# Kernel tuning notes

Hardware: AMD Instinct MI355X
Metric: run time of the kernel (lower is better)

Reference implementation:

```python
import jax, jax.numpy as jnp
import numpy as np

IMG_H, IMG_W = 512.0, 512.0
PRE_NMS = 2000   # training-mode pre_nms_top_n
POST_NMS = 2000  # training-mode post_nms_top_n
NMS_THRESH = 0.7
SCORE_THRESH = 0.0
MIN_SIZE = 0.001


def setup_inputs() -> dict:
    key = jax.random.key(0)
    k1, k2, k3 = jax.random.split(key, 3)
    N = 8
    num_anchors_per_level = (49152, 12288, 3072, 768, 192)  # strides 4..64, 3 anchors/loc on 512^2
    A = sum(num_anchors_per_level)
    cxy = jax.random.uniform(k1, (N, A, 2), minval=0.0, maxval=512.0)
    wh = jax.random.uniform(k2, (N, A, 2), minval=2.0, maxval=120.0)
    proposals = jnp.concatenate([cxy - wh / 2, cxy + wh / 2], axis=-1)  # xyxy
    objectness = jax.random.normal(k3, (N, A), dtype=jnp.float32)
    return {"proposals": proposals, "objectness": objectness,
            "num_anchors_per_level": num_anchors_per_level}


def _box_iou(a, b):
    # a: [K,4], b: [K,4] -> [K,K] pairwise IoU (torchvision box_iou semantics)
    area_a = (a[:, 2] - a[:, 0]) * (a[:, 3] - a[:, 1])
    area_b = (b[:, 2] - b[:, 0]) * (b[:, 3] - b[:, 1])
    lt = jnp.maximum(a[:, None, :2], b[None, :, :2])
    rb = jnp.minimum(a[:, None, 2:], b[None, :, 2:])
    wh = jnp.clip(rb - lt, 0.0)
    inter = wh[..., 0] * wh[..., 1]
    return inter / (area_a[:, None] + area_b[None, :] - inter)


def _per_image(boxes, scores, lvl):
    # boxes [K,4] xyxy, scores [K] (sigmoid probs), lvl [K] int32 level ids
    # 1) clip to image
    x = jnp.clip(boxes[:, 0::2], 0.0, IMG_W)
    y = jnp.clip(boxes[:, 1::2], 0.0, IMG_H)
    boxes = jnp.stack([x[:, 0], y[:, 0], x[:, 1], y[:, 1]], axis=-1)
    # 2) small-box + 3) score-threshold masks (masking instead of boolean indexing)
    ws = boxes[:, 2] - boxes[:, 0]
    hs = boxes[:, 3] - boxes[:, 1]
    valid = (ws >= MIN_SIZE) & (hs >= MIN_SIZE) & (scores >= SCORE_THRESH)
    # 4) batched NMS: offset boxes per level so levels never overlap
    off = lvl.astype(boxes.dtype) * (jnp.max(boxes) + 1.0)
    off_boxes = boxes + off[:, None]
    sm = jnp.where(valid, scores, -jnp.inf)
    order = jnp.argsort(-sm)                 # descending score, invalid last
    boxes_s = boxes[order]
    scores_s = scores[order]
    valid_s = valid[order]
    ob_s = jax.lax.stop_gradient(off_boxes[order])
    K = ob_s.shape[0]
    iou = _box_iou(ob_s, ob_s)               # [K,K], keep decision is non-differentiable
    j = jnp.arange(K)
    def body(i, keep):
        suppress = keep[i] & (iou[i] > NMS_THRESH) & (j > i)
        return keep & ~suppress
    keep = jax.lax.fori_loop(0, K, body, valid_s)
    # 5) top post_nms kept boxes, padded to fixed size with zeros
    rank = jnp.cumsum(keep.astype(jnp.int32)) - 1
    sel_key = jnp.where(keep & (rank < POST_NMS), rank, K)
    idx = jnp.argsort(sel_key)[:POST_NMS]
    out_valid = sel_key[idx] < K
    out_boxes = jnp.where(out_valid[:, None], boxes_s[idx], 0.0)
    out_scores = jnp.where(out_valid, scores_s[idx], 0.0)
    return out_boxes, out_scores


def _forward(proposals, objectness, num_anchors_per_level):
    N = proposals.shape[0]
    napl = [int(n) for n in num_anchors_per_level]
    # per-level, per-image top-k on objectness (get_top_n_idx)
    idx_list, lv_list, off = [], [], 0
    for i, n in enumerate(napl):
        k = min(PRE_NMS, n)
        _, ti = jax.lax.top_k(objectness[:, off:off + n], k)
        idx_list.append(ti + off)
        lv_list.append(jnp.full((k,), i, dtype=jnp.int32))
        off += n
    top_idx = jnp.concatenate(idx_list, axis=1)   # [N, K_total]
    lvls = jnp.concatenate(lv_list)               # [K_total], same for every image
    bidx = jnp.arange(N)[:, None]
    obj = objectness[bidx, top_idx]
    props = proposals[bidx, top_idx]
    scores = jax.nn.sigmoid(obj)
    return jax.vmap(lambda b, s: _per_image(b, s, lvls))(props, scores)


def reference(proposals, objectness, num_anchors_per_level):
    # returns (boxes [N, POST_NMS, 4], scores [N, POST_NMS]); invalid slots zero-padded
    return _forward(proposals, objectness, num_anchors_per_level)
```

## Files before the change

### kernel.cpp

```cpp
#include <hip/hip_runtime.h>
#include <math.h>

#define NIMG 8
#define ATOT 65472
#define KTOT 6960
#define POST 2000
#define TILES_PER_IMG 1668
#define NTILES (NIMG*TILES_PER_IMG)
#define ESEG 1024
#define M_TIE 0.7000000178813934326171875
#define PAD(i) ((i) + ((i) >> 5))
#define WAVE_SYNC() asm volatile("s_waitcnt lgkmcnt(0)" ::: "memory")

__constant__ int c_NAPL[5]  = {49152,12288,3072,768,192};
__constant__ int c_LOFF[5]  = {0,49152,61440,64512,65280};
__constant__ int c_KSEL[5]  = {2000,2000,2000,768,192};
__constant__ int c_CBASE[5] = {0,2000,4000,6000,6768};
__constant__ int c_GLVL[5]  = {32,32,32,12,3};
__constant__ int c_TILEPFX[6] = {0,528,1056,1584,1662,1668};

__device__ __forceinline__ unsigned f2u(float f){
  unsigned b = __float_as_uint(f);
  return (b & 0x80000000u) ? ~b : (b | 0x80000000u);
}
__device__ __forceinline__ unsigned long long mkkey(unsigned u, unsigned gidx){
  return ((unsigned long long)u << 32) | (unsigned long long)(0xFFFFFFFFu - gidx);
}
__device__ __forceinline__ unsigned long long shflx64(unsigned long long v, int m){
  int lo = __shfl_xor((int)(unsigned)v, m);
  int hi = __shfl_xor((int)(unsigned)(v >> 32), m);
  return ((unsigned long long)(unsigned)hi << 32) | (unsigned)lo;
}
__device__ __forceinline__ unsigned long long bstep(unsigned long long v, int elem,
                                                    int size, int st){
  unsigned long long p = shflx64(v, st);
  bool lower = (elem & st) == 0;
  bool desc  = (elem & size) == 0;
  bool takeMax = (lower == desc);
  bool gt = v > p;
  return (takeMax == gt) ? v : p;
}

extern "C" __global__ void __launch_bounds__(1024)
k_select(const float* __restrict__ prop, const float* __restrict__ obj,
         unsigned long long* __restrict__ cand, float4* __restrict__ cbox,
         unsigned* __restrict__ zzone){
  __shared__ unsigned long long sb[2112];
  __shared__ unsigned hist[4096];
  __shared__ unsigned scan[1024];
  __shared__ unsigned h8[256];
  __shared__ unsigned s_b12, s_cumAbove, s_t20, s_cnt;
  int task = blockIdx.x, img = task/5, lvl = task%5;
  int n = c_NAPL[lvl], k = c_KSEL[lvl], tid = threadIdx.x;
  if (task == 0)
    for (int i = tid; i < 1280; i += 1024) zzone[i] = 0u;

  const float4* o4 = (const float4*)(obj + (size_t)img*ATOT + c_LOFF[lvl]);
  int n4 = n >> 2;
  unsigned kk = (unsigned)k;
  unsigned T = 0u;
  if (k < n){
    for (int i = tid; i < 4096; i += 1024) hist[i] = 0u;
    if (tid < 256) h8[tid] = 0u;
    __syncthreads();
    for (int i = tid; i < n4; i += 1024){
      float4 v = o4[i];
      atomicAdd(&hist[f2u(v.x) >> 20], 1u);
      atomicAdd(&hist[f2u(v.y) >> 20], 1u);
      atomicAdd(&hist[f2u(v.z) >> 20], 1u);
      atomicAdd(&hist[f2u(v.w) >> 20], 1u);
    }
    __syncthreads();
    unsigned own[4]; unsigned s = 0;
    int b0 = tid*4;
    #pragma unroll
    for (int j = 0; j < 4; ++j){ own[j] = hist[b0+j]; s += own[j]; }
    scan[tid] = s;
    __syncthreads();
    for (int d = 1; d < 1024; d <<= 1){
      unsigned v = (tid + d < 1024) ? scan[tid + d] : 0u;
      __syncthreads();
      scan[tid] += v;
      __syncthreads();
    }
    {
      unsigned R = scan[tid] - s;
      unsigned sufn = R;
      #pragma unroll
      for (int j = 3; j >= 0; --j){
        unsigned sufj = sufn + own[j];
        if (sufj >= kk && sufn < kk){ s_b12 = (unsigned)(b0 + j); s_cumAbove = sufn; }
        sufn = sufj;
      }
    }
    __syncthreads();
    unsigned b12 = s_b12;
    for (int i = tid; i < n4; i += 1024){
      float4 v = o4[i];
      unsigned ux = f2u(v.x), uy = f2u(v.y), uz = f2u(v.z), uw = f2u(v.w);
      if ((ux >> 20) == b12) atomicAdd(&h8[(ux >> 12) & 255u], 1u);
      if ((uy >> 20) == b12) atomicAdd(&h8[(uy >> 12) & 255u], 1u);
      if ((uz >> 20) == b12) atomicAdd(&h8[(uz >> 12) & 255u], 1u);
      if ((uw >> 20) == b12) atomicAdd(&h8[(uw >> 12) & 255u], 1u);
    }
    __syncthreads();
    if (tid < 256) scan[tid] = h8[tid];
    __syncthreads();
    for (int d = 1; d < 256; d <<= 1){
      unsigned v = 0;
      if (tid < 256) v = (tid + d < 256) ? scan[tid + d] : 0u;
      __syncthreads();
      if (tid < 256) scan[tid] += v;
      __syncthreads();
    }
    if (tid < 256){
      unsigned sufj = s_cumAbove + scan[tid];
      unsigned sufn = s_cumAbove + ((tid < 255) ? scan[tid + 1] : 0u);
      if (sufj >= kk && sufn < kk) s_t20 = (s_b12 << 8) | (unsigned)tid;
    }
    __syncthreads();
    T = s_t20;
  }
  if (tid == 0) s_cnt = 0u;
  __syncthreads();
  int abase = c_LOFF[lvl];
  int lane = tid & 63, wv = tid >> 6;
  for (int i = tid; i < n4; i += 1024){
    float4 v = o4[i];
    float vv[4] = {v.x, v.y, v.z, v.w};
    #pragma unroll
    for (int c2 = 0; c2 < 4; ++c2){
      unsigned u = f2u(vv[c2]);
      bool pred = (u >> 12) >= T;
      unsigned long long bm = __ballot(pred);
      unsigned cw = (unsigned)__popcll(bm);
      unsigned basep = 0;
      if (lane == 0 && cw) basep = atomicAdd(&s_cnt, cw);
      basep = __shfl(basep, 0);
      if (pred){
        unsigned p = basep + (unsigned)__popcll(bm & ((1ull << lane) - 1ull));
        if (p < 2048u) sb[PAD(p)] = mkkey(u, (unsigned)(abase + i*4 + c2));
      }
    }
  }
  __syncthreads();
  int cnt = (int)min(s_cnt, 2048u);
  int m = 256; while (m < k || m < cnt) m <<= 1;
  for (int i = cnt + tid; i < m; i += 1024) sb[PAD(i)] = 0ull;
  __syncthreads();

  int elemA = (wv << 7) | lane, elemB = elemA | 64;
  bool active = (elemA < m);
  unsigned long long va = 0ull, vb = 0ull;
  if (active){ va = sb[PAD(elemA)]; vb = sb[PAD(elemB)]; }
  if (active){
    for (int size = 2; size <= 64; size <<= 1)
      for (int st = size >> 1; st >= 1; st >>= 1){
        va = bstep(va, elemA, size, st);
        vb = bstep(vb, elemB, size, st);
      }
    {
      bool desc = ((elemA & 128) == 0);
      unsigned long long mx = (va > vb) ? va : vb;
      unsigned long long mn = (va > vb) ? vb : va;
      va = desc ? mx : mn; vb = desc ? mn : mx;
      for (int st = 32; st >= 1; st >>= 1){
        va = bstep(va, elemA, 128, st);
        vb = bstep(vb, elemB, 128, st);
      }
    }
  }
  for (int S = 256; S <= m; S <<= 1){
    if (active){ sb[PAD(elemA)] = va; sb[PAD(elemB)] = vb; }
    __syncthreads();
    for (int st = S >> 1; st >= 128; st >>= 1){
      for (int t = tid; t < (m >> 1); t += 1024){
        int lo = t & (st - 1);
        int i  = ((t - lo) << 1) + lo;
        int j  = i + st;
        bool desc = ((i & S) == 0);
        unsigned long long x = sb[PAD(i)], y = sb[PAD(j)];
        if (desc ? (x < y) : (x > y)){ sb[PAD(i)] = y; sb[PAD(j)] = x; }
      }
      __syncthreads();
    }
    if (active){
      va = sb[PAD(elemA)]; vb = sb[PAD(elemB)];
      bool desc = ((elemA & S) == 0);
      unsigned long long mx = (va > vb) ? va : vb;
      unsigned long long mn = (va > vb) ? vb : va;
      va = desc ? mx : mn; vb = desc ? mn : mx;
      for (int st = 32; st >= 1; st >>= 1){
        va = bstep(va, elemA, S, st);
        vb = bstep(vb, elemB, S, st);
      }
    }
  }
  const float4* pr = (const float4*)(prop + (size_t)img*ATOT*4);
  size_t base = (size_t)img*KTOT + c_CBASE[lvl];
  if (active){
    if (elemA < k){
      cand[base + elemA] = va;
      unsigned gidx = 0xFFFFFFFFu - (unsigned)(va & 0xFFFFFFFFull);
      float4 p = pr[gidx];
      cbox[base + elemA] = make_float4(fminf(fmaxf(p.x,0.f),512.f), fminf(fmaxf(p.y,0.f),512.f),
                                       fminf(fmaxf(p.z,0.f),512.f), fminf(fmaxf(p.w,0.f),512.f));
    }
    if (elemB < k){
      cand[base + elemB] = vb;
      unsigned gidx = 0xFFFFFFFFu - (unsigned)(vb & 0xFFFFFFFFull);
      float4 p = pr[gidx];
      cbox[base + elemB] = make_float4(fminf(fmaxf(p.x,0.f),512.f), fminf(fmaxf(p.y,0.f),512.f),
                                       fminf(fmaxf(p.z,0.f),512.f), fminf(fmaxf(p.w,0.f),512.f));
    }
  }
}

extern "C" __global__ void __launch_bounds__(256)
k_mask(const float4* __restrict__ cbox, unsigned* __restrict__ ecnt,
       unsigned* __restrict__ eseg, float4* __restrict__ out4, int out_n4){
  __shared__ float4 colb[4][64];
  __shared__ float  colA[4][64];
  int tid = threadIdx.x, lane = tid & 63, wv = tid >> 6;
  int bid = blockIdx.x;
  if (bid < 79){
    int z = bid*256 + tid;
    if (z < out_n4) out4[z] = make_float4(0.f,0.f,0.f,0.f);
  }
  int tile = bid*4 + wv;
  int img = tile / TILES_PER_IMG, r = tile % TILES_PER_IMG;
  int lvl = 0;
  while (r >= c_TILEPFX[lvl + 1]) ++lvl;
  int t = r - c_TILEPFX[lvl];
  int G = c_GLVL[lvl], k = c_KSEL[lvl];
  int gi = 0;
  while (t >= G - gi){ t -= G - gi; ++gi; }
  int gj = gi + t;
  int task = img*5 + lvl;
  const float4* cb = cbox + (size_t)img*KTOT + c_CBASE[lvl];

  int jj = gj*64 + lane;
  float4 bb = (jj < k) ? cb[jj] : make_float4(0.f,0.f,0.f,0.f);
  colb[wv][lane] = bb;
  colA[wv][lane] = (bb.z - bb.x) * (bb.w - bb.y);
  WAVE_SYNC();

  int i = gi*64 + lane;
  unsigned long long word = 0ull, ambw = 0ull;
  float4 a = make_float4(0.f,0.f,0.f,0.f);
  float aarea = 0.f;
  if (i < k){
    a = cb[i];
    aarea = (a.z - a.x) * (a.w - a.y);
    #pragma unroll 8
    for (int j = 0; j < 64; ++j){
      float4 b = colb[wv][j];
      float ix = fminf(a.z, b.z) - fmaxf(a.x, b.x);
      float iy = fminf(a.w, b.w) - fmaxf(a.y, b.y);
      float inter = ix * iy;
      float uni = (aarea + colA[wv][j]) - inter;
      bool base = (ix > 0.f) & (iy > 0.f);
      bool hi  = inter >= 0.701f * uni;
      bool lo  = inter <  0.699f * uni;
      word |= (base & hi)              ? (1ull << j) : 0ull;
      ambw |= (base & (!hi) & (!lo))   ? (1ull << j) : 0ull;
    }
  }
  if (__any(ambw != 0ull)){
    unsigned long long aw = ambw;
    while (aw){
      int j = __ffsll(aw) - 1; aw &= aw - 1;
      float4 b = colb[wv][j];
      float ix = fminf(a.z, b.z) - fmaxf(a.x, b.x);
      float iy = fminf(a.w, b.w) - fmaxf(a.y, b.y);
      float inter = ix * iy;
      float uni = (aarea + colA[wv][j]) - inter;
      if ((double)inter >= M_TIE * (double)uni)
        word |= (1ull << j);
    }
  }
  if (gi == gj)
    word &= (lane == 63) ? 0ull : (~0ull << (lane + 1));

  int nb = __popcll(word);
  int pfx = nb;
  for (int d = 1; d < 64; d <<= 1){
    int v = __shfl_up(pfx, d);
    if (lane >= d) pfx += v;
  }
  int total = __shfl(pfx, 63);
  if (total > 0){
    unsigned base = 0;
    if (lane == 0) base = atomicAdd(&ecnt[task*32 + gi], (unsigned)total);
    base = __shfl(base, 0);
    unsigned idx = base + (unsigned)(pfx - nb);
    unsigned* ep = eseg + (size_t)(task*32 + gi)*ESEG;
    while (word){
      int j = __ffsll(word) - 1; word &= word - 1;
      if (idx < ESEG) ep[idx] = ((unsigned)i << 16) | (unsigned)(gj*64 + j);
      ++idx;
    }
  }
}

extern "C" __global__ void __launch_bounds__(256)
k_scan(const unsigned long long* __restrict__ cand, const unsigned* __restrict__ ecnt,
       const unsigned* __restrict__ eseg, unsigned long long* __restrict__ clist,
       unsigned* __restrict__ ccnt){
  __shared__ unsigned ledge[6144];
  __shared__ unsigned soff[33], wpfx[33];
  __shared__ unsigned long long sm[64];
  __shared__ unsigned long long remW[32], keepW[32];
  __shared__ unsigned long long s_hasI;
  int task = blockIdx.x, img = task / 5, lvl = task % 5;
  int k = c_KSEL[lvl], nW = c_GLVL[lvl], tid = threadIdx.x;

  if (tid == 0){
    unsigned s = 0;
    for (int w = 0; w < nW; ++w){ soff[w] = s; s += min(ecnt[task*32 + w], (unsigned)ESEG); }
    soff[nW] = s;
  }
  if (tid < 32) remW[tid] = 0ull;
  __syncthreads();
  for (int w = 0; w < nW; ++w){
    unsigned c = soff[w+1] - soff[w];
    const unsigned* ep = eseg + (size_t)(task*32 + w)*ESEG;
    for (unsigned e = tid; e < c; e += 256){
      unsigned p = soff[w] + e;
      if (p < 6144u) ledge[p] = ep[e];
    }
  }
  __syncthreads();

  if (tid < 64){
    int lane = tid;
    for (int w = 0; w < nW; ++w){
      unsigned c = soff[w+1] - soff[w];
      if (c == 0) continue;
      const unsigned* ep = eseg + (size_t)(task*32 + w)*ESEG;
      sm[lane] = 0ull;
      if (lane == 0) s_hasI = 0ull;
      WAVE_SYNC();
      for (unsigned e = lane; e < c; e += 64){
        unsigned p = soff[w] + e;
        unsigned ed = (p < 6144u) ? ledge[p] : ep[e];
        int i = (int)(ed >> 16), j = (int)(ed & 0xFFFFu);
        if ((j >> 6) == w){
          atomicOr(&sm[i & 63], 1ull << (j & 63));
          atomicOr(&s_hasI, 1ull << (i & 63));
        }
      }
      WAVE_SYNC();
      if (lane == 0){
        unsigned long long r = remW[w];
        unsigned long long x = s_hasI & ~r;
        while (x){
          int i = __ffsll(x) - 1;
          r |= sm[i];
          x &= ~(1ull << i);
          x &= ~r;
        }
        remW[w] = r;
      }
      WAVE_SYNC();
      unsigned long long keep_w = ~remW[w];
      for (unsigned e = lane; e < c; e += 64){
        unsigned p = soff[w] + e;
        unsigned ed = (p < 6144u) ? ledge[p] : ep[e];
        int i = (int)(ed >> 16), j = (int)(ed & 0xFFFFu), wj = j >> 6;
        if (wj != w && ((keep_w >> (i & 63)) & 1ull))
          atomicOr(&remW[wj], 1ull << (j & 63));
      }
      WAVE_SYNC();
    }
    if (lane < 32){
      unsigned long long v = 0ull;
      if (lane < nW){
        int rem = k - lane*64;
        v = (rem >= 64) ? ~0ull : ((1ull << rem) - 1ull);
      }
      keepW[lane] = v & ~remW[lane];
    }
    WAVE_SYNC();
    if (lane == 0){
      unsigned s = 0;
      for (int w = 0; w < nW; ++w){ wpfx[w] = s; s += (unsigned)__popcll(keepW[w]); }
      ccnt[task] = s;
    }
  }
  __syncthreads();
  size_t base = (size_t)img*KTOT + c_CBASE[lvl];
  for (int i = tid; i < k; i += 256){
    unsigned long long w = keepW[i >> 6];
    if ((w >> (i & 63)) & 1ull){
      unsigned long long lowmask = (i & 63) ? ((1ull << (i & 63)) - 1ull) : 0ull;
      unsigned rank = wpfx[i >> 6] + (unsigned)__popcll(w & lowmask);
      clist[base + rank] = cand[base + i];
    }
  }
}

__device__ __forceinline__ int cntGreater(const unsigned long long* base, int len,
                                          unsigned long long x){
  int lo = 0, hi = len;
  while (lo < hi){
    int mid = (lo + hi) >> 1;
    if (base[mid] > x) lo = mid + 1; else hi = mid;
  }
  return lo;
}

extern "C" __global__ void __launch_bounds__(1024)
k_merge(const float* __restrict__ prop, const float* __restrict__ obj,
        const unsigned long long* __restrict__ clist, const unsigned* __restrict__ ccnt,
        float* __restrict__ out){
  __shared__ unsigned long long keys[KTOT];
  __shared__ int loff[6], lcnt[5];
  int img = blockIdx.x >> 3, eighth = blockIdx.x & 7, tid = threadIdx.x;
  if (tid == 0){
    int s = 0;
    for (int l = 0; l < 5; ++l){ lcnt[l] = (int)ccnt[img*5 + l]; loff[l] = s; s += lcnt[l]; }
    loff[5] = s;
  }
  __syncthreads();
  for (int l = 0; l < 5; ++l){
    size_t gb = (size_t)img*KTOT + c_CBASE[l];
    int c = lcnt[l], lo = loff[l];
    for (int e = tid; e < c; e += 1024) keys[lo + e] = clist[gb + e];
  }
  __syncthreads();
  const float4* pr = (const float4*)(prop + (size_t)img*ATOT*4);
  const float*  o  = obj + (size_t)img*ATOT;
  float* ob = out + (size_t)img*POST*4;
  float* os = out + (size_t)NIMG*POST*4 + (size_t)img*POST;
  int tot = loff[5];
  for (int tt = tid; ; tt += 1024){
    int t = 8*tt + eighth;
    if (t >= tot) break;
    int lvl = 0;
    while (t >= loff[lvl + 1]) ++lvl;
    unsigned long long x = keys[t];
    int pos = t - loff[lvl];
    for (int l = 0; l < 5; ++l){
      if (l == lvl) continue;
      pos += cntGreater(keys + loff[l], lcnt[l], x);
    }
    if (pos < POST){
      unsigned gidx = 0xFFFFFFFFu - (unsigned)(x & 0xFFFFFFFFull);
      float4 p = pr[gidx];
      ob[pos*4 + 0] = fminf(fmaxf(p.x, 0.f), 512.f);
      ob[pos*4 + 1] = fminf(fmaxf(p.y, 0.f), 512.f);
      ob[pos*4 + 2] = fminf(fmaxf(p.z, 0.f), 512.f);
      ob[pos*4 + 3] = fminf(fmaxf(p.w, 0.f), 512.f);
      double sgm = 1.0 / (1.0 + exp(-(double)o[gidx]));
      os[pos] = (float)sgm;
    }
  }
}

extern "C" void kernel_launch(void* const* d_in, const int* in_sizes, int n_in,
                              void* d_out, int out_size, void* d_ws, size_t ws_size,
                              hipStream_t stream){
  const float* prop = (const float*)d_in[0];
  const float* obj  = (const float*)d_in[1];
  char* ws = (char*)d_ws;
  unsigned*           ecnt = (unsigned*)(ws);
  unsigned*           ccnt = (unsigned*)(ws + 5120);
  unsigned long long* cand = (unsigned long long*)(ws + 5632);
  unsigned long long* clist= (unsigned long long*)(ws + 451072);
  float4*             cbox = (float4*)(ws + 896512);
  unsigned*           eseg = (unsigned*)(ws + 1787392);

  int out_n4 = out_size / 4;
  hipLaunchKernelGGL(k_select, dim3(40),  dim3(1024), 0, stream, prop, obj, cand, cbox, ecnt);
  hipLaunchKernelGGL(k_mask,   dim3(NTILES/4), dim3(256), 0, stream, cbox, ecnt, eseg,
                     (float4*)d_out, out_n4);
  hipLaunchKernelGGL(k_scan,   dim3(40),  dim3(256),  0, stream, cand, ecnt, eseg, clist, ccnt);
  hipLaunchKernelGGL(k_merge,  dim3(64),  dim3(1024), 0, stream, prop, obj, clist, ccnt, (float*)d_out);
}
```

Measured before the change: 180.7 us.

## Split top-k threshold selection into sliced histogram kernels; use readlane in IoU mask

Replaces the single 40-block k_select, where one block histogrammed an entire 49k-element level, with three kernels. k_hist and k_refine spread the 12-bit and 8-bit radix histograms over 11 slices per image, k_b12 merges the slabs to find the bucket, and k_append finishes the threshold and appends candidates. This is meant to fix poor GPU occupancy in the selection phase, at the cost of three extra launches and global-memory histogram slabs. Separately, the IoU mask loop now broadcasts column boxes with readlane instead of reading LDS, and it is fully unrolled without a divergent i<k branch.

Measured after the change: 196.8 us. 1.09x slower.

```diff
diff --git a/kernel.cpp b/kernel.cpp
--- a/kernel.cpp
+++ b/kernel.cpp
@@ -8,6 +8,8 @@
 #define TILES_PER_IMG 1668
 #define NTILES (NIMG*TILES_PER_IMG)
 #define ESEG 1024
+#define SLICES_PER_IMG 11
+#define NSLICE (NIMG*SLICES_PER_IMG)
 #define M_TIE 0.7000000178813934326171875
 #define PAD(i) ((i) + ((i) >> 5))
 #define WAVE_SYNC() asm volatile("s_waitcnt lgkmcnt(0)" ::: "memory")
@@ -18,6 +20,10 @@
 __constant__ int c_CBASE[5] = {0,2000,4000,6000,6768};
 __constant__ int c_GLVL[5]  = {32,32,32,12,3};
 __constant__ int c_TILEPFX[6] = {0,528,1056,1584,1662,1668};
+__constant__ int c_SLVL[11]  = {0,0,0,0,0,0,0,0,1,1,2};
+__constant__ int c_SPART[11] = {0,1,2,3,4,5,6,7,0,1,0};
+__constant__ int c_SNP[3]    = {8,2,1};
+__constant__ int c_SBASE[3]  = {0,8,10};
 
 __device__ __forceinline__ unsigned f2u(float f){
   unsigned b = __float_as_uint(f);
@@ -40,16 +46,101 @@
   bool gt = v > p;
   return (takeMax == gt) ? v : p;
 }
+__device__ __forceinline__ float rdlane(float v, int j){
+  return __uint_as_float(__builtin_amdgcn_readlane(__float_as_uint(v), j));
+}
+
+extern "C" __global__ void __launch_bounds__(256)
+k_hist(const float* __restrict__ obj, unsigned* __restrict__ hslab){
+  __shared__ unsigned hist[4096];
+  int sid = blockIdx.x, img = sid / SLICES_PER_IMG, s = sid % SLICES_PER_IMG;
+  int tid = threadIdx.x;
+  int lvl = c_SLVL[s], part = c_SPART[s], np = c_SNP[lvl];
+  int n4 = c_NAPL[lvl] >> 2, chunk = n4 / np, c0 = part * chunk;
+  const float4* o4 = (const float4*)(obj + (size_t)img*ATOT + c_LOFF[lvl]);
+  for (int i = tid; i < 4096; i += 256) hist[i] = 0u;
+  __syncthreads();
+  for (int i = tid; i < chunk; i += 256){
+    float4 v = o4[c0 + i];
+    atomicAdd(&hist[f2u(v.x) >> 20], 1u);
+    atomicAdd(&hist[f2u(v.y) >> 20], 1u);
+    atomicAdd(&hist[f2u(v.z) >> 20], 1u);
+    atomicAdd(&hist[f2u(v.w) >> 20], 1u);
+  }
+  __syncthreads();
+  unsigned* out = hslab + (size_t)sid * 4096;
+  for (int i = tid; i < 4096; i += 256) out[i] = hist[i];
+}
 
 extern "C" __global__ void __launch_bounds__(1024)
-k_select(const float* __restrict__ prop, const float* __restrict__ obj,
+k_b12(const unsigned* __restrict__ hslab, unsigned* __restrict__ tinfo){
+  __shared__ unsigned scan[1024];
+  __shared__ unsigned s_b12, s_cum;
+  int b = blockIdx.x, img = b / 3, lvl = b % 3, tid = threadIdx.x;
+  int np = c_SNP[lvl], sb0 = img*SLICES_PER_IMG + c_SBASE[lvl];
+  unsigned kk = (unsigned)c_KSEL[lvl];
+  unsigned own[4]; unsigned ssum = 0;
+  int b0 = tid * 4;
+  #pragma unroll
+  for (int j = 0; j < 4; ++j){
+    unsigned v = 0;
+    for (int sl = 0; sl < np; ++sl) v += hslab[(size_t)(sb0 + sl)*4096 + b0 + j];
+    own[j] = v; ssum += v;
+  }
+  scan[tid] = ssum;
+  __syncthreads();
+  for (int d = 1; d < 1024; d <<= 1){
+    unsigned v = (tid + d < 1024) ? scan[tid + d] : 0u;
+    __syncthreads();
+    scan[tid] += v;
+    __syncthreads();
+  }
+  {
+    unsigned R = scan[tid] - ssum;
+    unsigned sufn = R;
+    #pragma unroll
+    for (int j = 3; j >= 0; --j){
+      unsigned sufj = sufn + own[j];
+      if (sufj >= kk && sufn < kk){ s_b12 = (unsigned)(b0 + j); s_cum = sufn; }
+      sufn = sufj;
+    }
+  }
+  __syncthreads();
+  if (tid == 0){ tinfo[b*2] = s_b12; tinfo[b*2 + 1] = s_cum; }
+}
+
+extern "C" __global__ void __launch_bounds__(256)
+k_refine(const float* __restrict__ obj, const unsigned* __restrict__ tinfo,
+         unsigned* __restrict__ h8slab){
+  __shared__ unsigned h8[256];
+  int sid = blockIdx.x, img = sid / SLICES_PER_IMG, s = sid % SLICES_PER_IMG;
+  int tid = threadIdx.x;
+  int lvl = c_SLVL[s], part = c_SPART[s], np = c_SNP[lvl];
+  int n4 = c_NAPL[lvl] >> 2, chunk = n4 / np, c0 = part * chunk;
+  unsigned b12 = tinfo[(img*3 + lvl)*2];
+  const float4* o4 = (const float4*)(obj + (size_t)img*ATOT + c_LOFF[lvl]);
+  h8[tid] = 0u;
+  __syncthreads();
+  for (int i = tid; i < chunk; i += 256){
+    float4 v = o4[c0 + i];
+    unsigned ux = f2u(v.x), uy = f2u(v.y), uz = f2u(v.z), uw = f2u(v.w);
+    if ((ux >> 20) == b12) atomicAdd(&h8[(ux >> 12) & 255u], 1u);
+    if ((uy >> 20) == b12) atomicAdd(&h8[(uy >> 12) & 255u], 1u);
+    if ((uz >> 20) == b12) atomicAdd(&h8[(uz >> 12) & 255u], 1u);
+    if ((uw >> 20) == b12) atomicAdd(&h8[(uw >> 12) & 255u], 1u);
+  }
+  __syncthreads();
+  h8slab[(size_t)sid*256 + tid] = h8[tid];
+}
+
+extern "C" __global__ void __launch_bounds__(1024)
+k_append(const float* __restrict__ prop, const float* __restrict__ obj,
+         const unsigned* __restrict__ tinfo, const unsigned* __restrict__ h8slab,
          unsigned long long* __restrict__ cand, float4* __restrict__ cbox,
          unsigned* __restrict__ zzone){
   __shared__ unsigned long long sb[2112];
-  __shared__ unsigned hist[4096];
-  __shared__ unsigned scan[1024];
-  __shared__ unsigned h8[256];
-  __shared__ unsigned s_b12, s_cumAbove, s_t20, s_cnt;
+  __shared__ unsigned scan[256];
+  __shared__ unsigned s_t20, s_cnt;
   int task = blockIdx.x, img = task/5, lvl = task%5;
   int n = c_NAPL[lvl], k = c_KSEL[lvl], tid = threadIdx.x;
   if (task == 0)
@@ -60,51 +151,14 @@
   unsigned kk = (unsigned)k;
   unsigned T = 0u;
   if (k < n){
-    for (int i = tid; i < 4096; i += 1024) hist[i] = 0u;
-    if (tid < 256) h8[tid] = 0u;
-    __syncthreads();
-    for (int i = tid; i < n4; i += 1024){
-      float4 v = o4[i];
-      atomicAdd(&hist[f2u(v.x) >> 20], 1u);
-      atomicAdd(&hist[f2u(v.y) >> 20], 1u);
-      atomicAdd(&hist[f2u(v.z) >> 20], 1u);
-      atomicAdd(&hist[f2u(v.w) >> 20], 1u);
-    }
-    __syncthreads();
-    unsigned own[4]; unsigned s = 0;
-    int b0 = tid*4;
-    #pragma unroll
-    for (int j = 0; j < 4; ++j){ own[j] = hist[b0+j]; s += own[j]; }
-    scan[tid] = s;
-    __syncthreads();
-    for (int d = 1; d < 1024; d <<= 1){
-      unsigned v = (tid + d < 1024) ? scan[tid + d] : 0u;
-      __syncthreads();
-      scan[tid] += v;
-      __syncthreads();
-    }
-    {
-      unsigned R = scan[tid] - s;
-      unsigned sufn = R;
-      #pragma unroll
-      for (int j = 3; j >= 0; --j){
-        unsigned sufj = sufn + own[j];
-        if (sufj >= kk && sufn < kk){ s_b12 = (unsigned)(b0 + j); s_cumAbove = sufn; }
-        sufn = sufj;
-      }
-    }
-    __syncthreads();
-    unsigned b12 = s_b12;
-    for (int i = tid; i < n4; i += 1024){
-      float4 v = o4[i];
-      unsigned ux = f2u(v.x), uy = f2u(v.y), uz = f2u(v.z), uw = f2u(v.w);
-      if ((ux >> 20) == b12) atomicAdd(&h8[(ux >> 12) & 255u], 1u);
-      if ((uy >> 20) == b12) atomicAdd(&h8[(uy >> 12) & 255u], 1u);
-      if ((uz >> 20) == b12) atomicAdd(&h8[(uz >> 12) & 255u], 1u);
-      if ((uw >> 20) == b12) atomicAdd(&h8[(uw >> 12) & 255u], 1u);
-    }
-    __syncthreads();
-    if (tid < 256) scan[tid] = h8[tid];
+    int tb = img*3 + lvl;
+    unsigned b12 = tinfo[tb*2], cum = tinfo[tb*2 + 1];
+    int np = c_SNP[lvl], sb0 = img*SLICES_PER_IMG + c_SBASE[lvl];
+    if (tid < 256){
+      unsigned v = 0;
+      for (int sl = 0; sl < np; ++sl) v += h8slab[(size_t)(sb0 + sl)*256 + tid];
+      scan[tid] = v;
+    }
     __syncthreads();
     for (int d = 1; d < 256; d <<= 1){
       unsigned v = 0;
@@ -114,9 +168,9 @@
       __syncthreads();
     }
     if (tid < 256){
-      unsigned sufj = s_cumAbove + scan[tid];
-      unsigned sufn = s_cumAbove + ((tid < 255) ? scan[tid + 1] : 0u);
-      if (sufj >= kk && sufn < kk) s_t20 = (s_b12 << 8) | (unsigned)tid;
+      unsigned sufj = cum + scan[tid];
+      unsigned sufn = cum + ((tid < 255) ? scan[tid + 1] : 0u);
+      if (sufj >= kk && sufn < kk) s_t20 = (b12 << 8) | (unsigned)tid;
     }
     __syncthreads();
     T = s_t20;
@@ -241,31 +295,31 @@
 
   int jj = gj*64 + lane;
   float4 bb = (jj < k) ? cb[jj] : make_float4(0.f,0.f,0.f,0.f);
+  float bAl = (bb.z - bb.x) * (bb.w - bb.y);
   colb[wv][lane] = bb;
-  colA[wv][lane] = (bb.z - bb.x) * (bb.w - bb.y);
+  colA[wv][lane] = bAl;
   WAVE_SYNC();
 
   int i = gi*64 + lane;
+  float4 a = cb[(i < k) ? i : (k - 1)];
+  float aarea = (a.z - a.x) * (a.w - a.y);
   unsigned long long word = 0ull, ambw = 0ull;
-  float4 a = make_float4(0.f,0.f,0.f,0.f);
-  float aarea = 0.f;
-  if (i < k){
-    a = cb[i];
-    aarea = (a.z - a.x) * (a.w - a.y);
-    #pragma unroll 8
-    for (int j = 0; j < 64; ++j){
-      float4 b = colb[wv][j];
-      float ix = fminf(a.z, b.z) - fmaxf(a.x, b.x);
-      float iy = fminf(a.w, b.w) - fmaxf(a.y, b.y);
-      float inter = ix * iy;
-      float uni = (aarea + colA[wv][j]) - inter;
-      bool base = (ix > 0.f) & (iy > 0.f);
-      bool hi  = inter >= 0.701f * uni;
-      bool lo  = inter <  0.699f * uni;
-      word |= (base & hi)              ? (1ull << j) : 0ull;
-      ambw |= (base & (!hi) & (!lo))   ? (1ull << j) : 0ull;
-    }
-  }
+  #pragma unroll
+  for (int j = 0; j < 64; ++j){
+    float bx = rdlane(bb.x, j), by = rdlane(bb.y, j);
+    float bz = rdlane(bb.z, j), bw = rdlane(bb.w, j);
+    float bA = rdlane(bAl, j);
+    float ix = fminf(a.z, bz) - fmaxf(a.x, bx);
+    float iy = fminf(a.w, bw) - fmaxf(a.y, by);
+    float inter = ix * iy;
+    float uni = (aarea + bA) - inter;
+    bool base = (ix > 0.f) & (iy > 0.f);
+    bool hi  = inter >= 0.701f * uni;
+    bool lo  = inter <  0.699f * uni;
+    word |= (base & hi)            ? (1ull << j) : 0ull;
+    ambw |= (base & (!hi) & (!lo)) ? (1ull << j) : 0ull;
+  }
+  if (i >= k){ word = 0ull; ambw = 0ull; }
   if (__any(ambw != 0ull)){
     unsigned long long aw = ambw;
     while (aw){
@@ -470,9 +524,16 @@
   unsigned long long* clist= (unsigned long long*)(ws + 451072);
   float4*             cbox = (float4*)(ws + 896512);
   unsigned*           eseg = (unsigned*)(ws + 1787392);
+  unsigned*           hslab  = (unsigned*)(ws + 1787392);
+  unsigned*           h8slab = (unsigned*)(ws + 1787392 + 1441792);
+  unsigned*           tinfo  = (unsigned*)(ws + 1787392 + 1441792 + 90112);
 
   int out_n4 = out_size / 4;
-  hipLaunchKernelGGL(k_select, dim3(40),  dim3(1024), 0, stream, prop, obj, cand, cbox, ecnt);
+  hipLaunchKernelGGL(k_hist,   dim3(NSLICE), dim3(256),  0, stream, obj, hslab);
+  hipLaunchKernelGGL(k_b12,    dim3(24),     dim3(1024), 0, stream, hslab, tinfo);
+  hipLaunchKernelGGL(k_refine, dim3(NSLICE), dim3(256),  0, stream, obj, tinfo, h8slab);
+  hipLaunchKernelGGL(k_append, dim3(40),     dim3(1024), 0, stream, prop, obj, tinfo,
+                     h8slab, cand, cbox, ecnt);
   hipLaunchKernelGGL(k_mask,   dim3(NTILES/4), dim3(256), 0, stream, cbox, ecnt, eseg,
                      (float4*)d_out, out_n4);
   hipLaunchKernelGGL(k_scan,   dim3(40),  dim3(256),  0, stream, cand, ecnt, eseg, clist, ccnt);
```
